# Optimization experiments

Hardware: AMD Instinct MI355X
Metric: run time of the kernel (lower is better)

Reference implementation:

```python
import jax, jax.numpy as jnp
import numpy as np

B, T, C, H = 4, 2048, 1024, 16
HD = C // H  # head_dim = 64


def setup_inputs() -> dict:
    key = jax.random.key(0)
    k1, k2, k3, k4, k5 = jax.random.split(key, 5)
    s = 1.0 / np.sqrt(C)
    return {
        "x": jax.random.normal(k1, (B, T, C), dtype=jnp.float32),
        "Wqkv": jax.random.normal(k2, (C, 3 * C), dtype=jnp.float32) * s,
        "bqkv": jnp.zeros((3 * C,), dtype=jnp.float32),
        "Wproj": jax.random.normal(k3, (C, C), dtype=jnp.float32) * s,
        "bproj": jnp.zeros((C,), dtype=jnp.float32),
    }


def reference(x, Wqkv, bqkv, Wproj, bproj):
    b, t, c = x.shape
    qkv = x @ Wqkv + bqkv                      # [B,T,3C]
    q, k, v = jnp.split(qkv, 3, axis=-1)
    # [B,T,C] -> [B,H,T,HD]
    q = q.reshape(b, t, H, HD).transpose(0, 2, 1, 3)
    k = k.reshape(b, t, H, HD).transpose(0, 2, 1, 3)
    v = v.reshape(b, t, H, HD).transpose(0, 2, 1, 3)
    att = jnp.einsum("bhqd,bhkd->bhqk", q, k) * (1.0 / np.sqrt(HD))
    causal = jnp.tril(jnp.ones((t, t), dtype=bool))
    att = jnp.where(causal[None, None], att, -jnp.inf)
    att = jax.nn.softmax(att, axis=-1)
    # dropout p=0.0 (eval) -> identity
    y = jnp.einsum("bhqk,bhkd->bhqd", att, v)  # [B,H,T,HD]
    y = y.transpose(0, 2, 1, 3).reshape(b, t, c)
    return y @ Wproj + bproj
```

## Files before the change

### kernel.cpp

```cpp
#include <hip/hip_runtime.h>


typedef unsigned short u16;
typedef short short8_t __attribute__((ext_vector_type(8)));
typedef float f32x4 __attribute__((ext_vector_type(4)));

#define B_ 4
#define T_ 2048
#define C_ 1024
#define H_ 16
#define HD_ 64
#define QSCALE 0.18033688011112042f

__device__ __forceinline__ u16 f32_to_bf16(float f) {
  unsigned int u = __float_as_uint(f);
  u += 0x7fffu + ((u >> 16) & 1u);
  return (u16)(u >> 16);
}

__device__ __forceinline__ void async_copy16(const void* g, void* l) {
  __builtin_amdgcn_global_load_lds((const __attribute__((address_space(1))) void*)g,
                                   (__attribute__((address_space(3))) void*)l, 16, 0, 0);
}

__device__ __forceinline__ void wave_barrier() { asm volatile("s_barrier" ::: "memory"); }
template <int N>
__device__ __forceinline__ void wait_vmcnt() {
  asm volatile("s_waitcnt vmcnt(%0)" ::"i"(N) : "memory");
}

__device__ __forceinline__ void transpose_tile(const float* __restrict__ in,
                                               u16* __restrict__ out, int K, int N, int bx, int by,
                                               float (*tile)[33], int tid) {
  int nb = bx * 32, kb = by * 32;
  int c = tid & 31, r0 = tid >> 5;
#pragma unroll
  for (int rr = 0; rr < 4; ++rr) {
    int r = r0 + rr * 8;
    tile[r][c] = in[(size_t)(kb + r) * N + nb + c];
  }
  __syncthreads();
#pragma unroll
  for (int rr = 0; rr < 4; ++rr) {
    int r = r0 + rr * 8;
    out[(size_t)(nb + r) * K + kb + c] = f32_to_bf16(tile[c][r]);
  }
}

__global__ void prep_kernel(const float* __restrict__ x, u16* __restrict__ Xb,
                            const float* __restrict__ Wqkv, u16* __restrict__ WqkvT,
                            const float* __restrict__ Wproj, u16* __restrict__ WprojT) {
  __shared__ float tile[32][33];
  int id = blockIdx.x;
  int tid = threadIdx.x;
  if (id < 8192) {
    int i = id * 256 + tid;
    float4 v = ((const float4*)x)[i];
    unsigned int a = (unsigned int)f32_to_bf16(v.x) | ((unsigned int)f32_to_bf16(v.y) << 16);
    unsigned int b = (unsigned int)f32_to_bf16(v.z) | ((unsigned int)f32_to_bf16(v.w) << 16);
    ((uint2*)Xb)[i] = make_uint2(a, b);
  } else if (id < 11264) {
    int t = id - 8192;
    transpose_tile(Wqkv, WqkvT, C_, 3 * C_, t % 96, t / 96, tile, tid);
  } else {
    int t = id - 11264;
    transpose_tile(Wproj, WprojT, C_, C_, t % 32, t / 32, tile, tid);
  }
}

__device__ __forceinline__ void stage_tile(const u16* __restrict__ A, const u16* __restrict__ Bt,
                                           int K, int m0, int n0, int k0, char* buf, int tid) {
#pragma unroll
  for (int it = 0; it < 2; ++it) {
    int j = it * 256 + tid;
    int row = j >> 2;
    int ch = ((j & 3) ^ (row >> 1)) & 3;
    async_copy16(A + (size_t)(m0 + row) * K + k0 + ch * 8, buf + j * 16);
    async_copy16(Bt + (size_t)(n0 + row) * K + k0 + ch * 8, buf + 8192 + j * 16);
  }
}

__device__ __forceinline__ void gemm_mainloop(const u16* __restrict__ A, const u16* __restrict__ Bt,
                                              int K, int m0, int n0, char* smem,
                                              f32x4 (&acc)[4][4]) {
  int tid = threadIdx.x;
  int lane = tid & 63, wave = tid >> 6;
  int quad = lane >> 4, l15 = lane & 15;
  int waveM = wave >> 1, waveN = wave & 1;
  int nIter = K >> 5;
  stage_tile(A, Bt, K, m0, n0, 0, smem, tid);
  stage_tile(A, Bt, K, m0, n0, 32, smem + 16384, tid);
  int cur = 0;
  for (int ki = 0; ki < nIter; ++ki) {
    int nxt2 = cur + 2;
    if (nxt2 >= 3) nxt2 -= 3;
    if (ki + 2 < nIter) {
      stage_tile(A, Bt, K, m0, n0, (ki + 2) << 5, smem + nxt2 * 16384, tid);
      wait_vmcnt<8>();
    } else if (ki + 2 == nIter) {
      wait_vmcnt<4>();
    } else {
      wait_vmcnt<0>();
    }
    wave_barrier();
    char* bufc = smem + cur * 16384;
    short8_t af[4], bfr[4];
#pragma unroll
    for (int mt = 0; mt < 4; ++mt) {
      int row = waveM * 64 + mt * 16 + l15;
      af[mt] = *(const short8_t*)(bufc + row * 64 + (((quad ^ (row >> 1)) & 3) << 4));
    }
#pragma unroll
    for (int nt = 0; nt < 4; ++nt) {
      int row = waveN * 64 + nt * 16 + l15;
      bfr[nt] = *(const short8_t*)(bufc + 8192 + row * 64 + (((quad ^ (row >> 1)) & 3) << 4));
    }
    __builtin_amdgcn_s_setprio(1);
#pragma unroll
    for (int mt = 0; mt < 4; ++mt)
#pragma unroll
      for (int nt = 0; nt < 4; ++nt)
        acc[mt][nt] = __builtin_amdgcn_mfma_f32_16x16x32_bf16(af[mt], bfr[nt], acc[mt][nt], 0, 0, 0);
    __builtin_amdgcn_s_setprio(0);
    wave_barrier();
    cur = cur + 1;
    if (cur == 3) cur = 0;
  }
}

__global__ __launch_bounds__(256, 3) void gemm1_kernel(const u16* __restrict__ A,
                                                       const u16* __restrict__ Bt,
                                                       const float* __restrict__ bias,
                                                       u16* __restrict__ Qo, u16* __restrict__ Ko,
                                                       u16* __restrict__ Vo) {
  __shared__ __align__(128) char smem[49152];
  f32x4 acc[4][4];
#pragma unroll
  for (int mt = 0; mt < 4; ++mt)
#pragma unroll
    for (int nt = 0; nt < 4; ++nt) acc[mt][nt] = (f32x4){0.f, 0.f, 0.f, 0.f};
  int m0 = blockIdx.y * 128, n0 = blockIdx.x * 128;
  gemm_mainloop(A, Bt, C_, m0, n0, smem, acc);

  int lane = threadIdx.x & 63, wave = threadIdx.x >> 6;
  int quad = lane >> 4, l15 = lane & 15;
  int waveM = wave >> 1, waveN = wave & 1;

  if (n0 < 2048) {
#pragma unroll
    for (int nt = 0; nt < 4; ++nt) {
      int n = n0 + waveN * 64 + nt * 16;
      int which = n >> 10;
      int rem = n & 1023;
      int head = rem >> 6;
      int d = (rem & 63) + l15;
      float bv = bias[n + l15];
      float sc = (which == 0) ? QSCALE : 1.0f;
      u16* dst = (which == 0) ? Qo : Ko;
#pragma unroll
      for (int mt = 0; mt < 4; ++mt) {
#pragma unroll
        for (int r = 0; r < 4; ++r) {
          int token = m0 + waveM * 64 + mt * 16 + quad * 4 + r;
          int b = token >> 11, t = token & 2047;
          dst[(((size_t)(b * H_ + head)) * T_ + t) * HD_ + d] =
              f32_to_bf16((acc[mt][nt][r] + bv) * sc);
        }
      }
    }
  } else {
    __syncthreads();
    char* W = smem + wave * 8192;
#pragma unroll
    for (int nt = 0; nt < 4; ++nt) {
      int nl = nt * 16 + l15;
      float bv = bias[n0 + waveN * 64 + nl];
#pragma unroll
      for (int mt = 0; mt < 4; ++mt) {
        int g = mt * 4 + quad;
        int pc = ((g >> 1) ^ (nl & 7)) & 7;
        uint2 pv;
        pv.x = (unsigned int)f32_to_bf16(acc[mt][nt][0] + bv) |
               ((unsigned int)f32_to_bf16(acc[mt][nt][1] + bv) << 16);
        pv.y = (unsigned int)f32_to_bf16(acc[mt][nt][2] + bv) |
               ((unsigned int)f32_to_bf16(acc[mt][nt][3] + bv) << 16);
        *(uint2*)(W + nl * 128 + pc * 16 + (g & 1) * 8) = pv;
      }
    }
    int b = m0 >> 11;
#pragma unroll
    for (int i = 0; i < 8; ++i) {
      int jj = i * 64 + lane;
      int nl = jj >> 3;
      int c = jj & 7;
      int pc = c ^ (nl & 7);
      uint4 v = *(const uint4*)(W + nl * 128 + pc * 16);
      int rem = (n0 - 2048) + waveN * 64 + nl;
      int head = rem >> 6, dd = rem & 63;
      int t0 = (m0 & 2047) + waveM * 64 + c * 8;
      *(uint4*)(Vo + ((size_t)(b * H_ + head) * HD_ + dd) * T_ + t0) = v;
    }
  }
}

__global__ __launch_bounds__(256, 3) void gemm2_kernel(const u16* __restrict__ A,
                                                       const u16* __restrict__ Bt,
                                                       const float* __restrict__ bias,
                                                       float* __restrict__ out) {
  __shared__ __align__(128) char smem[49152];
  f32x4 acc[4][4];
#pragma unroll
  for (int mt = 0; mt < 4; ++mt)
#pragma unroll
    for (int nt = 0; nt < 4; ++nt) acc[mt][nt] = (f32x4){0.f, 0.f, 0.f, 0.f};
  int m0 = blockIdx.y * 128, n0 = blockIdx.x * 128;
  gemm_mainloop(A, Bt, C_, m0, n0, smem, acc);

  int lane = threadIdx.x & 63, wave = threadIdx.x >> 6;
  int quad = lane >> 4, l15 = lane & 15;
  int waveM = wave >> 1, waveN = wave & 1;
#pragma unroll
  for (int nt = 0; nt < 4; ++nt) {
    int col = n0 + waveN * 64 + nt * 16 + l15;
    float bv = bias[col];
#pragma unroll
    for (int mt = 0; mt < 4; ++mt) {
#pragma unroll
      for (int r = 0; r < 4; ++r) {
        int token = m0 + waveM * 64 + mt * 16 + quad * 4 + r;
        out[(size_t)token * C_ + col] = acc[mt][nt][r] + bv;
      }
    }
  }
}

__device__ __forceinline__ void stage_kv(const u16* __restrict__ Kb, const u16* __restrict__ Vb,
                                         int kt, char* Ksb, char* Vsb, int tid) {
#pragma unroll
  for (int it = 0; it < 2; ++it) {
    int j = it * 256 + tid;
    int row = j >> 3;
    int ch = (j & 7) ^ (row & 7);
    async_copy16(Kb + (size_t)(kt * 64 + row) * HD_ + ch * 8, Ksb + j * 16);
    async_copy16(Vb + (size_t)row * T_ + kt * 64 + ch * 8, Vsb + j * 16);
  }
}

__global__ __launch_bounds__(256, 3) void attn_kernel(const u16* __restrict__ Qg,
                                                      const u16* __restrict__ Kg,
                                                      const u16* __restrict__ Vg,
                                                      u16* __restrict__ Yg) {
  __shared__ __align__(128) char smem[49152];
  int tid = threadIdx.x;
  int wave = tid >> 6, lane = tid & 63;
  int quad = lane >> 4, l15 = lane & 15;
  char* Psw = smem + 32768 + wave * 4096;
  int bh = blockIdx.x;
  int qt = 15 - blockIdx.y;
  int b = bh >> 4, h = bh & 15;
  const u16* Kb = Kg + (size_t)bh * T_ * HD_;
  const u16* Vb = Vg + (size_t)bh * HD_ * T_;

  short8_t qf[2][2];
#pragma unroll
  for (int mt = 0; mt < 2; ++mt)
#pragma unroll
    for (int ks = 0; ks < 2; ++ks) {
      int row = qt * 128 + wave * 32 + mt * 16 + l15;
      qf[mt][ks] = *(const short8_t*)(Qg + ((size_t)bh * T_ + row) * HD_ + ks * 32 + quad * 8);
    }

  stage_kv(Kb, Vb, 0, smem, smem + 16384, tid);

  float l_part[2][4];
  f32x4 o[2][4];
#pragma unroll
  for (int mt = 0; mt < 2; ++mt)
#pragma unroll
    for (int r = 0; r < 4; ++r) l_part[mt][r] = 0.f;
#pragma unroll
  for (int mt = 0; mt < 2; ++mt)
#pragma unroll
    for (int dt = 0; dt < 4; ++dt) o[mt][dt] = (f32x4){0.f, 0.f, 0.f, 0.f};

  int ktmax_blk = 2 * qt + 1;
  int ktmax_wave = 2 * qt + (wave >> 1);
  for (int kt = 0; kt <= ktmax_blk; ++kt) {
    int cur = kt & 1;
    char* Ksc = smem + cur * 8192;
    char* Vtc = smem + 16384 + cur * 8192;
    __syncthreads();
    if (kt < ktmax_blk)
      stage_kv(Kb, Vb, kt + 1, smem + (cur ^ 1) * 8192, smem + 16384 + (cur ^ 1) * 8192, tid);
    if (kt > ktmax_wave) continue;

    f32x4 s[2][4];
#pragma unroll
    for (int mt = 0; mt < 2; ++mt)
#pragma unroll
      for (int nt = 0; nt < 4; ++nt) s[mt][nt] = (f32x4){0.f, 0.f, 0.f, 0.f};
#pragma unroll
    for (int ks = 0; ks < 2; ++ks) {
      short8_t bfr[4];
#pragma unroll
      for (int nt = 0; nt < 4; ++nt) {
        int row = nt * 16 + l15;
        bfr[nt] = *(const short8_t*)(Ksc + row * 128 + ((((ks * 4 + quad) ^ row) & 7) << 4));
      }
#pragma unroll
      for (int mt = 0; mt < 2; ++mt)
#pragma unroll
        for (int nt = 0; nt < 4; ++nt)
          s[mt][nt] =
              __builtin_amdgcn_mfma_f32_16x16x32_bf16(qf[mt][ks], bfr[nt], s[mt][nt], 0, 0, 0);
    }

    if (kt == ktmax_wave) {
#pragma unroll
      for (int mt = 0; mt < 2; ++mt) {
        int qrow0 = qt * 128 + wave * 32 + mt * 16 + quad * 4;
#pragma unroll
        for (int nt = 0; nt < 4; ++nt) {
          int col = kt * 64 + nt * 16 + l15;
#pragma unroll
          for (int r = 0; r < 4; ++r) {
            float p = __builtin_amdgcn_exp2f(s[mt][nt][r]);
            if (col > qrow0 + r) p = 0.f;
            s[mt][nt][r] = p;
          }
        }
      }
    } else {
#pragma unroll
      for (int mt = 0; mt < 2; ++mt)
#pragma unroll
        for (int nt = 0; nt < 4; ++nt)
#pragma unroll
          for (int r = 0; r < 4; ++r) s[mt][nt][r] = __builtin_amdgcn_exp2f(s[mt][nt][r]);
    }

#pragma unroll
    for (int mt = 0; mt < 2; ++mt) {
#pragma unroll
      for (int r = 0; r < 4; ++r)
        l_part[mt][r] += (s[mt][0][r] + s[mt][1][r]) + (s[mt][2][r] + s[mt][3][r]);
#pragma unroll
      for (int nt = 0; nt < 4; ++nt) {
        int col = nt * 16 + l15;
#pragma unroll
        for (int r = 0; r < 4; ++r) {
          int prow = mt * 16 + quad * 4 + r;
          *(u16*)(Psw + prow * 128 + ((((col >> 3) ^ prow) & 7) << 4) + ((col & 7) << 1)) =
              (u16)(__float_as_uint(s[mt][nt][r]) >> 16);
        }
      }
    }

#pragma unroll
    for (int ks = 0; ks < 2; ++ks) {
      short8_t af[2], bfr[4];
#pragma unroll
      for (int mt = 0; mt < 2; ++mt) {
        int row = mt * 16 + l15;
        af[mt] = *(const short8_t*)(Psw + row * 128 + ((((ks * 4 + quad) ^ row) & 7) << 4));
      }
#pragma unroll
      for (int dt = 0; dt < 4; ++dt) {
        int row = dt * 16 + l15;
        bfr[dt] = *(const short8_t*)(Vtc + row * 128 + ((((ks * 4 + quad) ^ row) & 7) << 4));
      }
#pragma unroll
      for (int mt = 0; mt < 2; ++mt)
#pragma unroll
        for (int dt = 0; dt < 4; ++dt)
          o[mt][dt] = __builtin_amdgcn_mfma_f32_16x16x32_bf16(af[mt], bfr[dt], o[mt][dt], 0, 0, 0);
    }
  }

#pragma unroll
  for (int mt = 0; mt < 2; ++mt) {
#pragma unroll
    for (int r = 0; r < 4; ++r) {
      float lsum = l_part[mt][r];
#pragma unroll
      for (int off = 1; off < 16; off <<= 1) lsum += __shfl_xor(lsum, off);
      float inv = 1.0f / lsum;
#pragma unroll
      for (int dt = 0; dt < 4; ++dt) {
        int t = qt * 128 + wave * 32 + mt * 16 + quad * 4 + r;
        float val = o[mt][dt][r] * inv;
        Yg[((size_t)(b * T_ + t)) * C_ + h * HD_ + dt * 16 + l15] = f32_to_bf16(val);
      }
    }
  }
}

extern "C" void kernel_launch(void* const* d_in, const int* in_sizes, int n_in,
                              void* d_out, int out_size, void* d_ws, size_t ws_size,
                              hipStream_t stream) {
  (void)in_sizes; (void)n_in; (void)out_size; (void)ws_size;
  const float* x = (const float*)d_in[0];
  const float* Wqkv = (const float*)d_in[1];
  const float* bqkv = (const float*)d_in[2];
  const float* Wproj = (const float*)d_in[3];
  const float* bproj = (const float*)d_in[4];
  float* out = (float*)d_out;
  char* ws = (char*)d_ws;

  u16* Xb = (u16*)ws;
  u16* WqkvT = (u16*)(ws + 16777216);
  u16* WprojT = (u16*)(ws + 16777216 + 6291456);
  u16* Q = (u16*)(ws + 25165824);
  u16* K = Q + 8388608;
  u16* V = K + 8388608;
  u16* Y = Xb;

  prep_kernel<<<12288, 256, 0, stream>>>(x, Xb, Wqkv, WqkvT, Wproj, WprojT);
  gemm1_kernel<<<dim3(24, 64), 256, 0, stream>>>(Xb, WqkvT, bqkv, Q, K, V);
  attn_kernel<<<dim3(64, 16), 256, 0, stream>>>(Q, K, V, Y);
  gemm2_kernel<<<dim3(8, 64), 256, 0, stream>>>(Y, WprojT, bproj, out);
}
```

Before: 237.2 us.

## Switch attention to 32x32x16 MFMA with register-resident P via lane shuffles

Rewrites the attention inner loop to use 32x32x16 bf16 MFMA tiles. S is computed transposed (K as A operand) so each lane holds a query column, which lets the probability fragments be packed with v_cvt_pk_bf16 and swapped across half-waves with shuffles instead of round-tripping through LDS. This removes the per-wave P shared buffer, cutting LDS from 48KB to 32KB, and removes the scalar bf16 stores and reloads. In exchange it adds cross-lane shuffles, a more complex epilogue with per-row shuffles for the normalizer, and a different register footprint.

```diff
diff --git a/kernel.cpp b/kernel.cpp
--- a/kernel.cpp
+++ b/kernel.cpp
@@ -4,6 +4,8 @@
 typedef unsigned short u16;
 typedef short short8_t __attribute__((ext_vector_type(8)));
 typedef float f32x4 __attribute__((ext_vector_type(4)));
+typedef float f32x16 __attribute__((ext_vector_type(16)));
+typedef unsigned int u32x4 __attribute__((ext_vector_type(4)));
 
 #define B_ 4
 #define T_ 2048
@@ -27,6 +29,12 @@
 template <int N>
 __device__ __forceinline__ void wait_vmcnt() {
   asm volatile("s_waitcnt vmcnt(%0)" ::"i"(N) : "memory");
+}
+
+__device__ __forceinline__ unsigned int cvt_pk_bf16(float lo, float hi) {
+  unsigned int r;
+  asm("v_cvt_pk_bf16_f32 %0, %1, %2" : "=v"(r) : "v"(lo), "v"(hi));
+  return r;
 }
 
 __device__ __forceinline__ void transpose_tile(const float* __restrict__ in,
@@ -246,42 +254,71 @@
   }
 }
 
+__device__ __forceinline__ float softmax_block(f32x16& s, int kbase_g, bool diag, int qrow_g,
+                                               int hi) {
+  float lsum = 0.f;
+#pragma unroll
+  for (int r = 0; r < 16; ++r) {
+    float p = __builtin_amdgcn_exp2f(s[r]);
+    if (diag) {
+      int kpos = kbase_g + (r & 3) + 8 * (r >> 2) + 4 * hi;
+      if (kpos > qrow_g) p = 0.f;
+    }
+    s[r] = p;
+    lsum += p;
+  }
+  return lsum;
+}
+
+__device__ __forceinline__ void pack_pfrags(const f32x16& s, int hi, short8_t& f0, short8_t& f1) {
+  unsigned int pk[8], qk[8];
+#pragma unroll
+  for (int j = 0; j < 8; ++j) pk[j] = cvt_pk_bf16(s[2 * j], s[2 * j + 1]);
+#pragma unroll
+  for (int j = 0; j < 8; ++j) qk[j] = (unsigned int)__shfl_xor((int)pk[j], 32);
+  u32x4 w0, w1;
+  if (hi == 0) {
+    w0 = (u32x4){pk[0], pk[1], qk[0], qk[1]};
+    w1 = (u32x4){pk[4], pk[5], qk[4], qk[5]};
+  } else {
+    w0 = (u32x4){qk[2], qk[3], pk[2], pk[3]};
+    w1 = (u32x4){qk[6], qk[7], pk[6], pk[7]};
+  }
+  f0 = __builtin_bit_cast(short8_t, w0);
+  f1 = __builtin_bit_cast(short8_t, w1);
+}
+
+#define MFMA32(a, b, c) __builtin_amdgcn_mfma_f32_32x32x16_bf16(a, b, c, 0, 0, 0)
+
 __global__ __launch_bounds__(256, 3) void attn_kernel(const u16* __restrict__ Qg,
                                                       const u16* __restrict__ Kg,
                                                       const u16* __restrict__ Vg,
                                                       u16* __restrict__ Yg) {
-  __shared__ __align__(128) char smem[49152];
+  __shared__ __align__(128) char smem[32768];
   int tid = threadIdx.x;
   int wave = tid >> 6, lane = tid & 63;
-  int quad = lane >> 4, l15 = lane & 15;
-  char* Psw = smem + 32768 + wave * 4096;
+  int l31 = lane & 31, hi = lane >> 5;
   int bh = blockIdx.x;
   int qt = 15 - blockIdx.y;
   int b = bh >> 4, h = bh & 15;
   const u16* Kb = Kg + (size_t)bh * T_ * HD_;
   const u16* Vb = Vg + (size_t)bh * HD_ * T_;
-
-  short8_t qf[2][2];
-#pragma unroll
-  for (int mt = 0; mt < 2; ++mt)
-#pragma unroll
-    for (int ks = 0; ks < 2; ++ks) {
-      int row = qt * 128 + wave * 32 + mt * 16 + l15;
-      qf[mt][ks] = *(const short8_t*)(Qg + ((size_t)bh * T_ + row) * HD_ + ks * 32 + quad * 8);
-    }
+  int qrow = qt * 128 + wave * 32 + l31;
+
+  short8_t qf[4];
+#pragma unroll
+  for (int f = 0; f < 4; ++f)
+    qf[f] = *(const short8_t*)(Qg + ((size_t)bh * T_ + qrow) * HD_ + f * 16 + hi * 8);
 
   stage_kv(Kb, Vb, 0, smem, smem + 16384, tid);
 
-  float l_part[2][4];
-  f32x4 o[2][4];
-#pragma unroll
-  for (int mt = 0; mt < 2; ++mt)
-#pragma unroll
-    for (int r = 0; r < 4; ++r) l_part[mt][r] = 0.f;
-#pragma unroll
-  for (int mt = 0; mt < 2; ++mt)
-#pragma unroll
-    for (int dt = 0; dt < 4; ++dt) o[mt][dt] = (f32x4){0.f, 0.f, 0.f, 0.f};
+  float l_lane = 0.f;
+  f32x16 o0, o1;
+#pragma unroll
+  for (int i = 0; i < 16; ++i) {
+    o0[i] = 0.f;
+    o1[i] = 0.f;
+  }
 
   int ktmax_blk = 2 * qt + 1;
   int ktmax_wave = 2 * qt + (wave >> 1);
@@ -294,104 +331,50 @@
       stage_kv(Kb, Vb, kt + 1, smem + (cur ^ 1) * 8192, smem + 16384 + (cur ^ 1) * 8192, tid);
     if (kt > ktmax_wave) continue;
 
-    f32x4 s[2][4];
-#pragma unroll
-    for (int mt = 0; mt < 2; ++mt)
-#pragma unroll
-      for (int nt = 0; nt < 4; ++nt) s[mt][nt] = (f32x4){0.f, 0.f, 0.f, 0.f};
-#pragma unroll
-    for (int ks = 0; ks < 2; ++ks) {
-      short8_t bfr[4];
-#pragma unroll
-      for (int nt = 0; nt < 4; ++nt) {
-        int row = nt * 16 + l15;
-        bfr[nt] = *(const short8_t*)(Ksc + row * 128 + ((((ks * 4 + quad) ^ row) & 7) << 4));
-      }
-#pragma unroll
-      for (int mt = 0; mt < 2; ++mt)
-#pragma unroll
-        for (int nt = 0; nt < 4; ++nt)
-          s[mt][nt] =
-              __builtin_amdgcn_mfma_f32_16x16x32_bf16(qf[mt][ks], bfr[nt], s[mt][nt], 0, 0, 0);
-    }
-
-    if (kt == ktmax_wave) {
-#pragma unroll
-      for (int mt = 0; mt < 2; ++mt) {
-        int qrow0 = qt * 128 + wave * 32 + mt * 16 + quad * 4;
-#pragma unroll
-        for (int nt = 0; nt < 4; ++nt) {
-          int col = kt * 64 + nt * 16 + l15;
-#pragma unroll
-          for (int r = 0; r < 4; ++r) {
-            float p = __builtin_amdgcn_exp2f(s[mt][nt][r]);
-            if (col > qrow0 + r) p = 0.f;
-            s[mt][nt][r] = p;
-          }
-        }
-      }
-    } else {
-#pragma unroll
-      for (int mt = 0; mt < 2; ++mt)
-#pragma unroll
-        for (int nt = 0; nt < 4; ++nt)
-#pragma unroll
-          for (int r = 0; r < 4; ++r) s[mt][nt][r] = __builtin_amdgcn_exp2f(s[mt][nt][r]);
-    }
-
-#pragma unroll
-    for (int mt = 0; mt < 2; ++mt) {
-#pragma unroll
-      for (int r = 0; r < 4; ++r)
-        l_part[mt][r] += (s[mt][0][r] + s[mt][1][r]) + (s[mt][2][r] + s[mt][3][r]);
-#pragma unroll
-      for (int nt = 0; nt < 4; ++nt) {
-        int col = nt * 16 + l15;
-#pragma unroll
-        for (int r = 0; r < 4; ++r) {
-          int prow = mt * 16 + quad * 4 + r;
-          *(u16*)(Psw + prow * 128 + ((((col >> 3) ^ prow) & 7) << 4) + ((col & 7) << 1)) =
-              (u16)(__float_as_uint(s[mt][nt][r]) >> 16);
-        }
-      }
-    }
-
-#pragma unroll
-    for (int ks = 0; ks < 2; ++ks) {
-      short8_t af[2], bfr[4];
-#pragma unroll
-      for (int mt = 0; mt < 2; ++mt) {
-        int row = mt * 16 + l15;
-        af[mt] = *(const short8_t*)(Psw + row * 128 + ((((ks * 4 + quad) ^ row) & 7) << 4));
-      }
-#pragma unroll
-      for (int dt = 0; dt < 4; ++dt) {
-        int row = dt * 16 + l15;
-        bfr[dt] = *(const short8_t*)(Vtc + row * 128 + ((((ks * 4 + quad) ^ row) & 7) << 4));
-      }
-#pragma unroll
-      for (int mt = 0; mt < 2; ++mt)
-#pragma unroll
-        for (int dt = 0; dt < 4; ++dt)
-          o[mt][dt] = __builtin_amdgcn_mfma_f32_16x16x32_bf16(af[mt], bfr[dt], o[mt][dt], 0, 0, 0);
-    }
-  }
-
-#pragma unroll
-  for (int mt = 0; mt < 2; ++mt) {
-#pragma unroll
-    for (int r = 0; r < 4; ++r) {
-      float lsum = l_part[mt][r];
-#pragma unroll
-      for (int off = 1; off < 16; off <<= 1) lsum += __shfl_xor(lsum, off);
-      float inv = 1.0f / lsum;
-#pragma unroll
-      for (int dt = 0; dt < 4; ++dt) {
-        int t = qt * 128 + wave * 32 + mt * 16 + quad * 4 + r;
-        float val = o[mt][dt][r] * inv;
-        Yg[((size_t)(b * T_ + t)) * C_ + h * HD_ + dt * 16 + l15] = f32_to_bf16(val);
-      }
-    }
+    f32x16 s0, s1;
+#pragma unroll
+    for (int i = 0; i < 16; ++i) {
+      s0[i] = 0.f;
+      s1[i] = 0.f;
+    }
+    int swz7 = l31 & 7;
+#pragma unroll
+    for (int f = 0; f < 4; ++f) {
+      int pc = (((f * 2 + hi) ^ swz7) & 7) << 4;
+      short8_t kf0 = *(const short8_t*)(Ksc + l31 * 128 + pc);
+      short8_t kf1 = *(const short8_t*)(Ksc + (32 + l31) * 128 + pc);
+      s0 = MFMA32(kf0, qf[f], s0);
+      s1 = MFMA32(kf1, qf[f], s1);
+    }
+
+    bool diag = (kt == ktmax_wave);
+    l_lane += softmax_block(s0, kt * 64, diag, qrow, hi);
+    l_lane += softmax_block(s1, kt * 64 + 32, diag, qrow, hi);
+
+    short8_t pf0, pf1, pf2, pf3;
+    pack_pfrags(s0, hi, pf0, pf1);
+    pack_pfrags(s1, hi, pf2, pf3);
+
+#pragma unroll
+    for (int f = 0; f < 4; ++f) {
+      int pc = (((f * 2 + hi) ^ swz7) & 7) << 4;
+      short8_t va = *(const short8_t*)(Vtc + l31 * 128 + pc);
+      short8_t vb = *(const short8_t*)(Vtc + (32 + l31) * 128 + pc);
+      short8_t pf = (f == 0) ? pf0 : (f == 1) ? pf1 : (f == 2) ? pf2 : pf3;
+      o0 = MFMA32(pf, va, o0);
+      o1 = MFMA32(pf, vb, o1);
+    }
+  }
+
+  float lc = l_lane + __shfl_xor(l_lane, 32);
+#pragma unroll
+  for (int r = 0; r < 16; ++r) {
+    int q_r = (r & 3) + 8 * (r >> 2) + 4 * hi;
+    float inv = 1.0f / __shfl(lc, q_r);
+    int t = qt * 128 + wave * 32 + q_r;
+    size_t base = ((size_t)(b * T_ + t)) * C_ + h * HD_;
+    Yg[base + l31] = f32_to_bf16(o0[r] * inv);
+    Yg[base + 32 + l31] = f32_to_bf16(o1[r] * inv);
   }
 }
 
```

New measurement: 243.4 us. 2.6% more time.
